# Kernel optimization log

Hardware: AMD Instinct MI355X
Metric: run time of the kernel (lower is better)

Reference implementation:

```python
import jax, jax.numpy as jnp
import numpy as np

N_NODES = 10000   # graph size (pos/field tables, dense adjacency)
FEATS = 32        # node_feats
HEADS = 4         # n_heads
SAMPLES = 256     # n_samples (random mids per endpoint)
SENTINELS = 8     # n_sentinels
N_BATCH = 2048    # edges per forward batch
N_EDGES_G = 100000  # graph edges used to build dense adjacency buffer


def setup_inputs() -> dict:
    key = jax.random.key(0)
    ks = jax.random.split(key, 7)
    edge = jax.random.randint(ks[0], (N_BATCH, 2), 0, N_NODES)
    mid0 = jax.random.randint(ks[1], (HEADS, N_BATCH, SAMPLES), 0, N_NODES)
    mid1 = jax.random.randint(ks[2], (HEADS, N_BATCH, SAMPLES), 0, N_NODES)
    # learned parameters (torch: nn.Parameter(torch.rand(...)), ones*5)
    pos = jax.random.uniform(ks[3], (HEADS, N_NODES, FEATS), dtype=jnp.float32)
    field = jax.random.uniform(ks[4], (HEADS, N_NODES, FEATS), dtype=jnp.float32)
    uncertainty = jnp.ones((1, 1, 1), jnp.float32) * 5.0
    # dense adjacency buffer: -1 everywhere, +1 on (symmetrized) graph edges
    src_g = jax.random.randint(ks[5], (N_EDGES_G,), 0, N_NODES)
    dst_g = jax.random.randint(ks[6], (N_EDGES_G,), 0, N_NODES)
    edge_mat = -jnp.ones((N_NODES, N_NODES), jnp.float32)
    edge_mat = edge_mat.at[src_g, dst_g].set(1.0).at[dst_g, src_g].set(1.0)
    return {"edge": edge, "mid0": mid0, "mid1": mid1, "pos": pos,
            "field": field, "uncertainty": uncertainty, "edge_mat": edge_mat}


def reference(edge, mid0, mid1, pos, field, uncertainty, edge_mat):
    src, dst = edge[:, 0], edge[:, 1]
    h = jnp.arange(HEADS)[:, None, None]           # head index for gathers
    # gather sampled mid-node positions and form difference vectors
    srcdiff = pos[:, src][:, :, None, :] - pos[h, mid0]   # (H, n, S, F)
    dstdiff = pos[:, dst][:, :, None, :] - pos[h, mid1]   # (H, n, S, F)
    # per-sample dot-product logits + memory bias (memory == -1 branch)
    logits1 = (jnp.einsum('hnsf,hnf->hns', srcdiff, field[:, dst])
               + uncertainty * edge_mat[mid0, dst[None, :, None]])
    logits2 = (jnp.einsum('hnsf,hnf->hns', dstdiff, field[:, src])
               + uncertainty * edge_mat[src[None, :, None], mid1])
    logits = jnp.concatenate([logits1, logits2], axis=2)  # (H, n, 2S)
    dist = jnp.concatenate([jnp.linalg.norm(srcdiff, axis=3),
                            jnp.linalg.norm(dstdiff, axis=3)], axis=2)
    # sentinels: zero logits at unit distance
    n = edge.shape[0]
    logits = jnp.concatenate([logits, jnp.zeros((HEADS, n, SENTINELS), logits.dtype)], axis=2)
    dist = jnp.concatenate([dist, jnp.ones((HEADS, n, SENTINELS), dist.dtype)], axis=2)
    # softmin aggregation: softmax over (1 - dist), weighted sum of logits, mean over heads
    w = jax.nn.softmax(1.0 - dist, axis=2)                # (H, n, 2S+sent)
    return jnp.sum(logits * w, axis=2).mean(0)            # (n,)
```

## Files before the change

### kernel.cpp

```cpp
#include <hip/hip_runtime.h>

#define N_NODES 10000
#define FEATS 32
#define HEADS 4
#define SAMPLES 256
#define N_BATCH 2048
#define CHUNK 64
#define NCHUNK ((2 * SAMPLES) / CHUNK)
#define NGROUP 40
#define NWORDS (NGROUP * 4)

__device__ __forceinline__ void gload_lds16(const float* g, float* l) {
    __builtin_amdgcn_global_load_lds(
        (const __attribute__((address_space(1))) void*)g,
        (__attribute__((address_space(3))) void*)l,
        16, 0, 0);
}

__global__ __launch_bounds__(256) void mask_kernel(
    const int* __restrict__ edge,
    const float* __restrict__ edge_mat,
    unsigned long long* __restrict__ ws_mask,
    float* __restrict__ out)
{
    const int n    = blockIdx.x;
    const int tid  = threadIdx.x;
    const int wave = tid >> 6;
    const int lane = tid & 63;

    const int src = edge[2 * n];
    const int dst = edge[2 * n + 1];
    if (tid == 0) out[n] = 0.f;

    unsigned long long* wsn = ws_mask + (size_t)n * 2 * NWORDS;

    #pragma unroll
    for (int r = 0; r < 2; ++r) {
        const float* rp = edge_mat + (size_t)(r ? src : dst) * N_NODES;
        for (int g = wave; g < NGROUP; g += 4) {
            int base = g * 256 + lane * 4;
            float4 v = make_float4(-1.f, -1.f, -1.f, -1.f);
            if (base < N_NODES) v = *(const float4*)(rp + base);
            unsigned long long b0 = __ballot(v.x > 0.f);
            unsigned long long b1 = __ballot(v.y > 0.f);
            unsigned long long b2 = __ballot(v.z > 0.f);
            unsigned long long b3 = __ballot(v.w > 0.f);
            if (lane < 4) {
                unsigned long long b = lane == 0 ? b0 : lane == 1 ? b1
                                     : lane == 2 ? b2 : b3;
                wsn[r * NWORDS + g * 4 + lane] = b;
            }
        }
    }
}

__global__ __launch_bounds__(64) void madgraph_kernel(
    const int* __restrict__ edge,
    const int* __restrict__ mid0,
    const int* __restrict__ mid1,
    const float* __restrict__ pos,
    const float* __restrict__ field,
    const float* __restrict__ unc,
    const unsigned long long* __restrict__ ws_mask,
    float* __restrict__ out)
{
    const int i    = blockIdx.x;
    const int h    = i & 3;
    const int n    = i >> 2;
    const int lane = threadIdx.x;

    __shared__ float s_rows[CHUNK][FEATS];
    __shared__ unsigned long long s_mask[2 * NWORDS];

    const int src = edge[2 * n];
    const int dst = edge[2 * n + 1];
    const float U = unc[0];

    const unsigned long long* wsn = ws_mask + (size_t)n * 2 * NWORDS;
    #pragma unroll
    for (int w = 0; w < 2 * NWORDS / 64; ++w)
        s_mask[w * 64 + lane] = wsn[w * 64 + lane];
    __syncthreads();

    const int qsrc = (lane & 7) ^ (lane >> 3);

    float4 A[8], F[8];
    float num = 0.f, den = 0.f;

    for (int c = 0; c < NCHUNK; ++c) {
        const int side = c >> 2;
        if (c == 0 || c == 4) {
            const float* pa = pos   + ((size_t)h * N_NODES + (side ? dst : src)) * FEATS;
            const float* pf = field + ((size_t)h * N_NODES + (side ? src : dst)) * FEATS;
            #pragma unroll
            for (int q = 0; q < 8; ++q) {
                A[q] = ((const float4*)pa)[q];
                F[q] = ((const float4*)pf)[q];
            }
        }
        const int* mids = side ? mid1 : mid0;
        const size_t sbase = ((size_t)h * N_BATCH + n) * SAMPLES + (c & 3) * CHUNK;
        const int m_own = mids[sbase + lane];

        #pragma unroll
        for (int t = 0; t < 8; ++t) {
            int row  = t * 8 + (lane >> 3);
            int mrow = __shfl(m_own, row);
            const float* gsrc = pos + ((size_t)h * N_NODES + mrow) * FEATS + qsrc * 4;
            gload_lds16(gsrc, &s_rows[t * 8][0]);
        }

        const unsigned long long wbits =
            s_mask[side * NWORDS + ((m_own >> 8) << 2) + (m_own & 3)];
        const float em = ((wbits >> ((m_own >> 2) & 63)) & 1ull) ? U : -U;

        asm volatile("s_waitcnt vmcnt(0)" ::: "memory");
        __builtin_amdgcn_sched_barrier(0);

        float dot = 0.f, nrm = 0.f;
        #pragma unroll
        for (int q = 0; q < 8; ++q) {
            int s = q ^ (lane & 7);
            float4 b = *(const float4*)&s_rows[lane][s * 4];
            float4 a = A[q], fv = F[q];
            float dx = a.x - b.x, dy = a.y - b.y, dz = a.z - b.z, dw = a.w - b.w;
            dot += dx * fv.x + dy * fv.y + dz * fv.z + dw * fv.w;
            nrm += dx * dx + dy * dy + dz * dz + dw * dw;
        }

        float logit = dot + em;
        float dist  = sqrtf(nrm);
        float e     = __expf(1.0f - dist);
        num += logit * e;
        den += e;
    }

    #pragma unroll
    for (int off = 32; off > 0; off >>= 1) {
        num += __shfl_xor(num, off);
        den += __shfl_xor(den, off);
    }
    if (lane == 0) {
        atomicAdd(out + n, 0.25f * (num / (den + 8.0f)));
    }
}

extern "C" void kernel_launch(void* const* d_in, const int* in_sizes, int n_in,
                              void* d_out, int out_size, void* d_ws, size_t ws_size,
                              hipStream_t stream) {
    const int*   edge     = (const int*)  d_in[0];
    const int*   mid0     = (const int*)  d_in[1];
    const int*   mid1     = (const int*)  d_in[2];
    const float* pos      = (const float*)d_in[3];
    const float* field    = (const float*)d_in[4];
    const float* unc      = (const float*)d_in[5];
    const float* edge_mat = (const float*)d_in[6];
    float*       out      = (float*)d_out;
    unsigned long long* ws_mask = (unsigned long long*)d_ws;

    mask_kernel<<<N_BATCH, 256, 0, stream>>>(edge, edge_mat, ws_mask, out);
    madgraph_kernel<<<N_BATCH * HEADS, 64, 0, stream>>>(edge, mid0, mid1, pos,
                                                        field, unc, ws_mask, out);
}
```

Measured before the change: 69.48 us.

## Double-buffer LDS gathers and prefetch next chunk's mid indices

Splits the LDS row buffer into two halves so the gather for chunk c+1 is issued before computing chunk c, using partial vmcnt waits. Mid indices are prefetched two chunks ahead and both sides' anchor/field rows are loaded up front. The loop is fully unrolled. This aims to hide global gather latency, at the cost of more registers and LDS per block and hand-tuned wait counts that must match the issued load count.

```diff
diff --git a/kernel.cpp b/kernel.cpp
--- a/kernel.cpp
+++ b/kernel.cpp
@@ -6,7 +6,7 @@
 #define SAMPLES 256
 #define N_BATCH 2048
 #define CHUNK 64
-#define NCHUNK ((2 * SAMPLES) / CHUNK)
+#define NCHUNK 8
 #define NGROUP 40
 #define NWORDS (NGROUP * 4)
 
@@ -54,7 +54,7 @@
     }
 }
 
-__global__ __launch_bounds__(64) void madgraph_kernel(
+__global__ __launch_bounds__(64, 2) void madgraph_kernel(
     const int* __restrict__ edge,
     const int* __restrict__ mid0,
     const int* __restrict__ mid1,
@@ -69,7 +69,7 @@
     const int n    = i >> 2;
     const int lane = threadIdx.x;
 
-    __shared__ float s_rows[CHUNK][FEATS];
+    __shared__ float s_rows[2][CHUNK][FEATS];
     __shared__ unsigned long long s_mask[2 * NWORDS];
 
     const int src = edge[2 * n];
@@ -80,49 +80,67 @@
     #pragma unroll
     for (int w = 0; w < 2 * NWORDS / 64; ++w)
         s_mask[w * 64 + lane] = wsn[w * 64 + lane];
-    __syncthreads();
 
+    float4 A[2][8], F[2][8];
+    #pragma unroll
+    for (int sd = 0; sd < 2; ++sd) {
+        const float* pa = pos   + ((size_t)h * N_NODES + (sd ? dst : src)) * FEATS;
+        const float* pf = field + ((size_t)h * N_NODES + (sd ? src : dst)) * FEATS;
+        #pragma unroll
+        for (int q = 0; q < 8; ++q) {
+            A[sd][q] = ((const float4*)pa)[q];
+            F[sd][q] = ((const float4*)pf)[q];
+        }
+    }
+
+    const size_t sb = ((size_t)h * N_BATCH + n) * SAMPLES;
+    int mc = mid0[sb + lane];
+    int mn = mid0[sb + 64 + lane];
     const int qsrc = (lane & 7) ^ (lane >> 3);
 
-    float4 A[8], F[8];
+    asm volatile("" ::: "memory");
+
+    #pragma unroll
+    for (int t = 0; t < 8; ++t) {
+        int mrow = __shfl(mc, t * 8 + (lane >> 3));
+        gload_lds16(pos + ((size_t)h * N_NODES + mrow) * FEATS + qsrc * 4,
+                    &s_rows[0][t * 8][0]);
+    }
+
     float num = 0.f, den = 0.f;
 
+    #pragma unroll
     for (int c = 0; c < NCHUNK; ++c) {
         const int side = c >> 2;
-        if (c == 0 || c == 4) {
-            const float* pa = pos   + ((size_t)h * N_NODES + (side ? dst : src)) * FEATS;
-            const float* pf = field + ((size_t)h * N_NODES + (side ? src : dst)) * FEATS;
+
+        if (c < 7) {
             #pragma unroll
-            for (int q = 0; q < 8; ++q) {
-                A[q] = ((const float4*)pa)[q];
-                F[q] = ((const float4*)pf)[q];
+            for (int t = 0; t < 8; ++t) {
+                int mrow = __shfl(mn, t * 8 + (lane >> 3));
+                gload_lds16(pos + ((size_t)h * N_NODES + mrow) * FEATS + qsrc * 4,
+                            &s_rows[(c + 1) & 1][t * 8][0]);
             }
         }
-        const int* mids = side ? mid1 : mid0;
-        const size_t sbase = ((size_t)h * N_BATCH + n) * SAMPLES + (c & 3) * CHUNK;
-        const int m_own = mids[sbase + lane];
+        int mn2 = 0;
+        if (c < 6) {
+            const int* mids2 = ((c + 2) >> 2) ? mid1 : mid0;
+            mn2 = mids2[sb + ((c + 2) & 3) * 64 + lane];
+        }
+        const unsigned long long wbits =
+            s_mask[side * NWORDS + ((mc >> 8) << 2) + (mc & 3)];
+        const float em = ((wbits >> ((mc >> 2) & 63)) & 1ull) ? U : -U;
 
-        #pragma unroll
-        for (int t = 0; t < 8; ++t) {
-            int row  = t * 8 + (lane >> 3);
-            int mrow = __shfl(m_own, row);
-            const float* gsrc = pos + ((size_t)h * N_NODES + mrow) * FEATS + qsrc * 4;
-            gload_lds16(gsrc, &s_rows[t * 8][0]);
-        }
-
-        const unsigned long long wbits =
-            s_mask[side * NWORDS + ((m_own >> 8) << 2) + (m_own & 3)];
-        const float em = ((wbits >> ((m_own >> 2) & 63)) & 1ull) ? U : -U;
-
-        asm volatile("s_waitcnt vmcnt(0)" ::: "memory");
+        if (c <= 5)      asm volatile("s_waitcnt vmcnt(9)" ::: "memory");
+        else if (c == 6) asm volatile("s_waitcnt vmcnt(8)" ::: "memory");
+        else             asm volatile("s_waitcnt vmcnt(0)" ::: "memory");
         __builtin_amdgcn_sched_barrier(0);
 
         float dot = 0.f, nrm = 0.f;
         #pragma unroll
         for (int q = 0; q < 8; ++q) {
             int s = q ^ (lane & 7);
-            float4 b = *(const float4*)&s_rows[lane][s * 4];
-            float4 a = A[q], fv = F[q];
+            float4 b = *(const float4*)&s_rows[c & 1][lane][s * 4];
+            float4 a = A[side][q], fv = F[side][q];
             float dx = a.x - b.x, dy = a.y - b.y, dz = a.z - b.z, dw = a.w - b.w;
             dot += dx * fv.x + dy * fv.y + dz * fv.z + dw * fv.w;
             nrm += dx * dx + dy * dy + dz * dz + dw * dw;
@@ -133,6 +151,8 @@
         float e     = __expf(1.0f - dist);
         num += logit * e;
         den += e;
+
+        mc = mn; mn = mn2;
     }
 
     #pragma unroll
```

Measured after the change: 75.93 us. +9.3%, slower.

## Double-buffer mid-row gathers and split each sample across lane pairs

Applied to the files above, without the earlier changes.

The main kernel now handles 32 samples per step, with two lanes per sample each covering half the features, then combines the halves with a lane shuffle. The next 32 mid-node rows are gathered into a second LDS buffer while the current buffer is being computed, so gather latency overlaps with math. All mid indices and the endpoint rows are loaded up front, and the endpoint registers are halved. Because both lanes of a pair add the same weight, num and den are doubled, and the sentinel term becomes 16 to match. This adds shuffles and relies on hand-counted vmcnt waits being correct.

```diff
diff --git a/kernel.cpp b/kernel.cpp
--- a/kernel.cpp
+++ b/kernel.cpp
@@ -5,8 +5,6 @@
 #define HEADS 4
 #define SAMPLES 256
 #define N_BATCH 2048
-#define CHUNK 64
-#define NCHUNK ((2 * SAMPLES) / CHUNK)
 #define NGROUP 40
 #define NWORDS (NGROUP * 4)
 
@@ -69,7 +67,7 @@
     const int n    = i >> 2;
     const int lane = threadIdx.x;
 
-    __shared__ float s_rows[CHUNK][FEATS];
+    __shared__ float s_rows[2][32][FEATS];
     __shared__ unsigned long long s_mask[2 * NWORDS];
 
     const int src = edge[2 * n];
@@ -80,59 +78,94 @@
     #pragma unroll
     for (int w = 0; w < 2 * NWORDS / 64; ++w)
         s_mask[w * 64 + lane] = wsn[w * 64 + lane];
-    __syncthreads();
+
+    const float* posh   = pos   + (size_t)h * N_NODES * FEATS;
+    const float* fieldh = field + (size_t)h * N_NODES * FEATS;
+
+    const int p = lane >> 1;
+    const int e = lane & 1;
+
+    float4 Ao[4], Fo[4];
+    {
+        const float* pa = posh   + (size_t)src * FEATS;
+        const float* pf = fieldh + (size_t)dst * FEATS;
+        #pragma unroll
+        for (int k = 0; k < 4; ++k) {
+            Ao[k] = ((const float4*)pa)[e * 4 + k];
+            Fo[k] = ((const float4*)pf)[e * 4 + k];
+        }
+    }
+
+    const size_t sb = ((size_t)h * N_BATCH + n) * SAMPLES;
+    int mm[8];
+    #pragma unroll
+    for (int c = 0; c < 8; ++c)
+        mm[c] = (c < 4 ? mid0 : mid1)[sb + (c & 3) * 64 + lane];
 
     const int qsrc = (lane & 7) ^ (lane >> 3);
 
-    float4 A[8], F[8];
+    asm volatile("s_waitcnt vmcnt(0) lgkmcnt(0)" ::: "memory");
+    __builtin_amdgcn_sched_barrier(0);
+
+    #pragma unroll
+    for (int t = 0; t < 4; ++t) {
+        int rid = __shfl(mm[0], t * 8 + (lane >> 3));
+        gload_lds16(posh + (size_t)rid * FEATS + qsrc * 4, &s_rows[0][t * 8][0]);
+    }
+
     float num = 0.f, den = 0.f;
 
-    for (int c = 0; c < NCHUNK; ++c) {
-        const int side = c >> 2;
-        if (c == 0 || c == 4) {
-            const float* pa = pos   + ((size_t)h * N_NODES + (side ? dst : src)) * FEATS;
-            const float* pf = field + ((size_t)h * N_NODES + (side ? src : dst)) * FEATS;
+    #pragma unroll
+    for (int hc = 0; hc < 16; ++hc) {
+        const int c    = hc >> 1;
+        const int side = hc >> 3;
+
+        if (hc == 8) {
+            const float* pa = posh   + (size_t)dst * FEATS;
+            const float* pf = fieldh + (size_t)src * FEATS;
             #pragma unroll
-            for (int q = 0; q < 8; ++q) {
-                A[q] = ((const float4*)pa)[q];
-                F[q] = ((const float4*)pf)[q];
+            for (int k = 0; k < 4; ++k) {
+                Ao[k] = ((const float4*)pa)[e * 4 + k];
+                Fo[k] = ((const float4*)pf)[e * 4 + k];
             }
         }
-        const int* mids = side ? mid1 : mid0;
-        const size_t sbase = ((size_t)h * N_BATCH + n) * SAMPLES + (c & 3) * CHUNK;
-        const int m_own = mids[sbase + lane];
 
-        #pragma unroll
-        for (int t = 0; t < 8; ++t) {
-            int row  = t * 8 + (lane >> 3);
-            int mrow = __shfl(m_own, row);
-            const float* gsrc = pos + ((size_t)h * N_NODES + mrow) * FEATS + qsrc * 4;
-            gload_lds16(gsrc, &s_rows[t * 8][0]);
+        if (hc < 15) {
+            const int c1 = (hc + 1) >> 1, hf1 = (hc + 1) & 1;
+            #pragma unroll
+            for (int t = 0; t < 4; ++t) {
+                int rid = __shfl(mm[c1], hf1 * 32 + t * 8 + (lane >> 3));
+                gload_lds16(posh + (size_t)rid * FEATS + qsrc * 4,
+                            &s_rows[(hc + 1) & 1][t * 8][0]);
+            }
         }
 
+        const int m = __shfl(mm[c], (hc & 1) * 32 + p);
         const unsigned long long wbits =
-            s_mask[side * NWORDS + ((m_own >> 8) << 2) + (m_own & 3)];
-        const float em = ((wbits >> ((m_own >> 2) & 63)) & 1ull) ? U : -U;
+            s_mask[side * NWORDS + ((m >> 8) << 2) + (m & 3)];
+        const float em = ((wbits >> ((m >> 2) & 63)) & 1ull) ? U : -U;
 
-        asm volatile("s_waitcnt vmcnt(0)" ::: "memory");
+        if (hc < 15) asm volatile("s_waitcnt vmcnt(4)" ::: "memory");
+        else         asm volatile("s_waitcnt vmcnt(0)" ::: "memory");
         __builtin_amdgcn_sched_barrier(0);
 
-        float dot = 0.f, nrm = 0.f;
+        float dh = 0.f, nh = 0.f;
         #pragma unroll
-        for (int q = 0; q < 8; ++q) {
-            int s = q ^ (lane & 7);
-            float4 b = *(const float4*)&s_rows[lane][s * 4];
-            float4 a = A[q], fv = F[q];
+        for (int k = 0; k < 4; ++k) {
+            const int s = (e * 4 + k) ^ (p & 7);
+            float4 b = *(const float4*)&s_rows[hc & 1][p][s * 4];
+            float4 a = Ao[k], fv = Fo[k];
             float dx = a.x - b.x, dy = a.y - b.y, dz = a.z - b.z, dw = a.w - b.w;
-            dot += dx * fv.x + dy * fv.y + dz * fv.z + dw * fv.w;
-            nrm += dx * dx + dy * dy + dz * dz + dw * dw;
+            dh += dx * fv.x + dy * fv.y + dz * fv.z + dw * fv.w;
+            nh += dx * dx + dy * dy + dz * dz + dw * dw;
         }
+        float dot = dh + __shfl_xor(dh, 1);
+        float nrm = nh + __shfl_xor(nh, 1);
 
         float logit = dot + em;
-        float dist  = sqrtf(nrm);
-        float e     = __expf(1.0f - dist);
-        num += logit * e;
-        den += e;
+        float wgt   = __expf(1.0f - sqrtf(nrm));
+        num += logit * wgt;
+        den += wgt;
     }
 
     #pragma unroll
@@ -141,7 +174,7 @@
         den += __shfl_xor(den, off);
     }
     if (lane == 0) {
-        atomicAdd(out + n, 0.25f * (num / (den + 8.0f)));
+        atomicAdd(out + n, 0.25f * (num / (den + 16.0f)));
     }
 }
 
```

After: 71.93 us. 3.5% more time.

## Gather mid-node rows directly to registers with 4-lane split per sample

Applied to the files above, without the earlier changes.

Replaces the per-chunk global-to-LDS staging and its full vmcnt wait with direct float4 loads into registers. Each group of 4 lanes handles one sampled row, and partial dot products and norms are combined with xor shuffles. The chunk loop is fully unrolled and all mid indices are prefetched so many gathers can be in flight at once. Blocks now hold 4 waves, each for a different edge. Because each sample's contribution is counted four times across its lane group, the sentinel constant is scaled to 32 to compensate. The cost is extra shuffles and redundant per-lane exp/sqrt work.

```diff
diff --git a/kernel.cpp b/kernel.cpp
--- a/kernel.cpp
+++ b/kernel.cpp
@@ -5,17 +5,8 @@
 #define HEADS 4
 #define SAMPLES 256
 #define N_BATCH 2048
-#define CHUNK 64
-#define NCHUNK ((2 * SAMPLES) / CHUNK)
 #define NGROUP 40
 #define NWORDS (NGROUP * 4)
-
-__device__ __forceinline__ void gload_lds16(const float* g, float* l) {
-    __builtin_amdgcn_global_load_lds(
-        (const __attribute__((address_space(1))) void*)g,
-        (__attribute__((address_space(3))) void*)l,
-        16, 0, 0);
-}
 
 __global__ __launch_bounds__(256) void mask_kernel(
     const int* __restrict__ edge,
@@ -54,7 +45,7 @@
     }
 }
 
-__global__ __launch_bounds__(64) void madgraph_kernel(
+__global__ __launch_bounds__(256) void madgraph_kernel(
     const int* __restrict__ edge,
     const int* __restrict__ mid0,
     const int* __restrict__ mid1,
@@ -64,13 +55,14 @@
     const unsigned long long* __restrict__ ws_mask,
     float* __restrict__ out)
 {
-    const int i    = blockIdx.x;
-    const int h    = i & 3;
-    const int n    = i >> 2;
-    const int lane = threadIdx.x;
+    const int b    = blockIdx.x;
+    const int h    = b & 3;
+    const int tid  = threadIdx.x;
+    const int w    = tid >> 6;
+    const int lane = tid & 63;
+    const int n    = (b >> 2) + 512 * w;
 
-    __shared__ float s_rows[CHUNK][FEATS];
-    __shared__ unsigned long long s_mask[2 * NWORDS];
+    __shared__ unsigned long long s_mask[4][2 * NWORDS];
 
     const int src = edge[2 * n];
     const int dst = edge[2 * n + 1];
@@ -78,61 +70,70 @@
 
     const unsigned long long* wsn = ws_mask + (size_t)n * 2 * NWORDS;
     #pragma unroll
-    for (int w = 0; w < 2 * NWORDS / 64; ++w)
-        s_mask[w * 64 + lane] = wsn[w * 64 + lane];
-    __syncthreads();
+    for (int k = 0; k < 5; ++k)
+        s_mask[w][k * 64 + lane] = wsn[k * 64 + lane];
 
-    const int qsrc = (lane & 7) ^ (lane >> 3);
+    const float* posh   = pos   + (size_t)h * N_NODES * FEATS;
+    const float* fieldh = field + (size_t)h * N_NODES * FEATS;
 
-    float4 A[8], F[8];
+    const int q = lane & 3;
+    const int g = lane >> 2;
+
+    float4 A[2][2], F[2][2];
+    #pragma unroll
+    for (int sd = 0; sd < 2; ++sd) {
+        const float4* pa = (const float4*)(posh   + (size_t)(sd ? dst : src) * FEATS);
+        const float4* pf = (const float4*)(fieldh + (size_t)(sd ? src : dst) * FEATS);
+        A[sd][0] = pa[q];
+        A[sd][1] = pa[q + 4];
+        F[sd][0] = pf[q];
+        F[sd][1] = pf[q + 4];
+    }
+
+    const size_t sb = ((size_t)h * N_BATCH + n) * SAMPLES;
+    int mm[8];
+    #pragma unroll
+    for (int c = 0; c < 8; ++c)
+        mm[c] = (c < 4 ? mid0 : mid1)[sb + (c & 3) * 64 + lane];
+
     float num = 0.f, den = 0.f;
 
-    for (int c = 0; c < NCHUNK; ++c) {
+    #pragma unroll
+    for (int c = 0; c < 8; ++c) {
         const int side = c >> 2;
-        if (c == 0 || c == 4) {
-            const float* pa = pos   + ((size_t)h * N_NODES + (side ? dst : src)) * FEATS;
-            const float* pf = field + ((size_t)h * N_NODES + (side ? src : dst)) * FEATS;
-            #pragma unroll
-            for (int q = 0; q < 8; ++q) {
-                A[q] = ((const float4*)pa)[q];
-                F[q] = ((const float4*)pf)[q];
+        #pragma unroll
+        for (int t = 0; t < 4; ++t) {
+            const int m = __shfl(mm[c], t * 16 + g);
+            const float4* rp = (const float4*)(posh + (size_t)m * FEATS);
+            float4 b0 = rp[q];
+            float4 b1 = rp[q + 4];
+
+            float dh = 0.f, nh = 0.f;
+            {
+                float4 a = A[side][0], f = F[side][0];
+                float dx = a.x - b0.x, dy = a.y - b0.y,
+                      dz = a.z - b0.z, dw = a.w - b0.w;
+                dh += dx * f.x + dy * f.y + dz * f.z + dw * f.w;
+                nh += dx * dx + dy * dy + dz * dz + dw * dw;
             }
+            {
+                float4 a = A[side][1], f = F[side][1];
+                float dx = a.x - b1.x, dy = a.y - b1.y,
+                      dz = a.z - b1.z, dw = a.w - b1.w;
+                dh += dx * f.x + dy * f.y + dz * f.z + dw * f.w;
+                nh += dx * dx + dy * dy + dz * dz + dw * dw;
+            }
+            dh += __shfl_xor(dh, 1); nh += __shfl_xor(nh, 1);
+            dh += __shfl_xor(dh, 2); nh += __shfl_xor(nh, 2);
+
+            const unsigned long long wbits =
+                s_mask[w][side * NWORDS + ((m >> 8) << 2) + (m & 3)];
+            const float em = ((wbits >> ((m >> 2) & 63)) & 1ull) ? U : -U;
+
+            const float wgt = __expf(1.0f - sqrtf(nh));
+            num += (dh + em) * wgt;
+            den += wgt;
         }
-        const int* mids = side ? mid1 : mid0;
-        const size_t sbase = ((size_t)h * N_BATCH + n) * SAMPLES + (c & 3) * CHUNK;
-        const int m_own = mids[sbase + lane];
-
-        #pragma unroll
-        for (int t = 0; t < 8; ++t) {
-            int row  = t * 8 + (lane >> 3);
-            int mrow = __shfl(m_own, row);
-            const float* gsrc = pos + ((size_t)h * N_NODES + mrow) * FEATS + qsrc * 4;
-            gload_lds16(gsrc, &s_rows[t * 8][0]);
-        }
-
-        const unsigned long long wbits =
-            s_mask[side * NWORDS + ((m_own >> 8) << 2) + (m_own & 3)];
-        const float em = ((wbits >> ((m_own >> 2) & 63)) & 1ull) ? U : -U;
-
-        asm volatile("s_waitcnt vmcnt(0)" ::: "memory");
-        __builtin_amdgcn_sched_barrier(0);
-
-        float dot = 0.f, nrm = 0.f;
-        #pragma unroll
-        for (int q = 0; q < 8; ++q) {
-            int s = q ^ (lane & 7);
-            float4 b = *(const float4*)&s_rows[lane][s * 4];
-            float4 a = A[q], fv = F[q];
-            float dx = a.x - b.x, dy = a.y - b.y, dz = a.z - b.z, dw = a.w - b.w;
-            dot += dx * fv.x + dy * fv.y + dz * fv.z + dw * fv.w;
-            nrm += dx * dx + dy * dy + dz * dz + dw * dw;
-        }
-
-        float logit = dot + em;
-        float dist  = sqrtf(nrm);
-        float e     = __expf(1.0f - dist);
-        num += logit * e;
-        den += e;
     }
 
     #pragma unroll
@@ -141,7 +142,7 @@
         den += __shfl_xor(den, off);
     }
     if (lane == 0) {
-        atomicAdd(out + n, 0.25f * (num / (den + 8.0f)));
+        atomicAdd(out + n, 0.25f * (num / (den + 32.0f)));
     }
 }
 
@@ -159,6 +160,6 @@
     unsigned long long* ws_mask = (unsigned long long*)d_ws;
 
     mask_kernel<<<N_BATCH, 256, 0, stream>>>(edge, edge_mat, ws_mask, out);
-    madgraph_kernel<<<N_BATCH * HEADS, 64, 0, stream>>>(edge, mid0, mid1, pos,
-                                                        field, unc, ws_mask, out);
+    madgraph_kernel<<<N_BATCH, 256, 0, stream>>>(edge, mid0, mid1, pos,
+                                                 field, unc, ws_mask, out);
 }
```

New measurement: 64.50 us. 7.2% less time.
